# Kernel optimization log

Hardware: AMD Instinct MI355X
Metric: run time of the kernel (lower is better)

Reference implementation:

```python
import jax, jax.numpy as jnp
import numpy as np
import math

D_MODEL = 512
NUM_HEADS = 8
B, L = 2, 4096
EPS_NORM = 1e-8
PLASTICITY = 1.0


def setup_inputs() -> dict:
    key = jax.random.key(0)
    ks = jax.random.split(key, 6)
    D, H = D_MODEL, NUM_HEADS
    std = 1.0 / math.sqrt(D)
    x = jax.random.normal(ks[0], (B, L, D), dtype=jnp.float32)
    qkv_w = jax.random.normal(ks[1], (3 * D, D), dtype=jnp.float32) * std
    qkv_b = jnp.zeros((3 * D,), dtype=jnp.float32)
    out_w = jax.random.normal(ks[2], (D, D), dtype=jnp.float32) * std
    out_b = jnp.zeros((D,), dtype=jnp.float32)
    decay_w = jax.random.normal(ks[3], (H, D), dtype=jnp.float32) * 0.02
    decay_b = jnp.full((H,), 4.0, dtype=jnp.float32)
    norm_scale = jnp.ones((D,), dtype=jnp.float32)
    return {"x": x, "qkv_w": qkv_w, "qkv_b": qkv_b, "out_w": out_w,
            "out_b": out_b, "decay_w": decay_w, "decay_b": decay_b,
            "norm_scale": norm_scale}


def _hebbian_forward(x, qkv_w, qkv_b, out_w, out_b, decay_w, decay_b, norm_scale):
    Bsz, Lsz, D = x.shape
    H = NUM_HEADS
    E = D // H
    # QKV projection (torch Linear: y = x @ W.T + b)
    qkv = x @ qkv_w.T + qkv_b
    q, k, v = jnp.split(qkv, 3, axis=-1)
    q = q.reshape(Bsz, Lsz, H, E)
    k = k.reshape(Bsz, Lsz, H, E)
    v = v.reshape(Bsz, Lsz, H, E)
    # feature map: elu(x) + 1
    q = (jax.nn.elu(q) + 1.0) / math.sqrt(E)
    k = jax.nn.elu(k) + 1.0
    # input-dependent decay per head
    decay_logits = x @ decay_w.T + decay_b          # (B,L,H)
    lambdas = (0.9 + 0.1 * jax.nn.sigmoid(decay_logits)) * PLASTICITY
    log_lambdas = jnp.log(jnp.clip(lambdas, 1e-6))[..., None]   # (B,L,H,1)
    log_lambda_cum = jnp.clip(jnp.cumsum(log_lambdas, axis=1), -50.0, 50.0)
    decay_k = jnp.exp(-log_lambda_cum)
    decay_q = jnp.exp(log_lambda_cum)
    k_decayed = k * decay_k
    q_decayed = q * decay_q
    # outer-product memory state cumsum: (B,L,H,E,E)
    kv = jnp.einsum('blhe,blhf->blhef', k_decayed, v)
    memory_state = jnp.cumsum(kv, axis=1)
    k_sum_decayed = jnp.cumsum(k_decayed, axis=1)
    num = jnp.einsum('blhe,blhef->blhf', q_decayed, memory_state)
    den = jnp.einsum('blhe,blhe->blh', q_decayed, k_sum_decayed)[..., None] + 1e-6
    out = (num / den).reshape(Bsz, Lsz, D)
    out = out @ out_w.T + out_b
    # RMSNorm (dropout is identity in eval)
    rnorm = jax.lax.rsqrt(jnp.mean(out * out, axis=-1, keepdims=True) + EPS_NORM)
    return out * rnorm * norm_scale


def reference(x, qkv_w, qkv_b, out_w, out_b, decay_w, decay_b, norm_scale):
    return _hebbian_forward(x, qkv_w, qkv_b, out_w, out_b, decay_w, decay_b, norm_scale)
```

## Files before the change

### kernel.cpp

```cpp
#include <hip/hip_runtime.h>

typedef unsigned short u16;
typedef unsigned int u32;

#define B_ 2
#define L_ 4096
#define D_ 512
#define H_ 8
#define E_ 64
#define M_ (B_*L_)
#define TD (3*D_)
#define NCH (L_/64)
#define BH (B_*H_)

typedef short bf16x8 __attribute__((ext_vector_type(8)));
typedef float f32x4 __attribute__((ext_vector_type(4)));

__device__ __forceinline__ float bf2f(u16 u){ return __uint_as_float(((u32)u)<<16); }
__device__ __forceinline__ u16 f2bf(float f){
  u32 u = __float_as_uint(f);
  u32 r = u + 0x7FFFu + ((u>>16)&1u);
  return (u16)(r>>16);
}
__device__ __forceinline__ float elu1(float v){ return v>0.f ? v+1.f : __expf(v); }

__device__ __forceinline__ void async_ld16(const u16* g, u16* l){
  __builtin_amdgcn_global_load_lds(
      (const __attribute__((address_space(1))) void*)g,
      (__attribute__((address_space(3))) void*)l, 16, 0, 0);
}

__global__ __launch_bounds__(256) void decay_conv_kernel(const float* __restrict__ x,
    const float* __restrict__ dw, const float* __restrict__ db,
    const float* __restrict__ qw, const float* __restrict__ ow,
    float* __restrict__ ll, u16* __restrict__ xb,
    u16* __restrict__ qwb, u16* __restrict__ owb)
{
  int blk = blockIdx.x;
  if (blk < 2048){
    int wv = threadIdx.x>>6, lane = threadIdx.x&63;
    int m = ((blk&7)<<10) + ((blk>>3)<<2) + wv;
    float xr[8];
    #pragma unroll
    for (int i=0;i<8;i++) xr[i] = x[(size_t)m*D_ + lane + 64*i];
    #pragma unroll
    for (int i=0;i<8;i++) xb[(size_t)m*D_ + lane + 64*i] = f2bf(xr[i]);
    int b = m >> 12, l = m & (L_-1);
    float acc8[8];
    #pragma unroll
    for (int h=0; h<8; h++){
      float a = 0.f;
      #pragma unroll
      for (int i=0;i<8;i++) a += xr[i]*dw[h*D_ + lane + 64*i];
      acc8[h] = a;
    }
    float s4[4];
    #pragma unroll
    for (int i=0;i<4;i++){
      float a = acc8[2*i], bb = acc8[2*i+1];
      bool odd = lane & 1;
      float keep = odd ? bb : a;
      float send = odd ? a : bb;
      s4[i] = keep + __shfl_xor(send, 1);
    }
    float s2[2];
    #pragma unroll
    for (int j=0;j<2;j++){
      float a = s4[2*j], bb = s4[2*j+1];
      bool sel = (lane>>1) & 1;
      float keep = sel ? bb : a;
      float send = sel ? a : bb;
      s2[j] = keep + __shfl_xor(send, 2);
    }
    float r;
    {
      bool sel = (lane>>2) & 1;
      float keep = sel ? s2[1] : s2[0];
      float send = sel ? s2[0] : s2[1];
      r = keep + __shfl_xor(send, 4);
    }
    r += __shfl_xor(r, 8);
    r += __shfl_xor(r, 16);
    r += __shfl_xor(r, 32);
    if (lane < 8){
      float z = r + db[lane];
      float lam = 0.9f + 0.1f/(1.f + __expf(-z));
      ll[((b*H_+lane)*L_) + l] = __logf(lam);
    }
  } else {
    int gid = (blk-2048)*256 + threadIdx.x;
    const float* src; u16* dst; int off;
    if (gid < 196608){ src = qw; dst = qwb; off = gid; }
    else { src = ow; dst = owb; off = gid - 196608; }
    float4 v = ((const float4*)src)[off];
    ushort4 o; o.x=f2bf(v.x); o.y=f2bf(v.y); o.z=f2bf(v.z); o.w=f2bf(v.w);
    ((ushort4*)dst)[off] = o;
  }
}

__global__ __launch_bounds__(256) void scan_kernel(const float* __restrict__ ll,
    float* __restrict__ cb)
{
  int bh = blockIdx.x, t = threadIdx.x;
  int lane = t & 63, wv = t >> 6;
  const float* p = ll + (size_t)bh*L_ + t*16;
  float s[16];
  #pragma unroll
  for (int q=0;q<4;q++){
    float4 v = *(const float4*)(p + q*4);
    s[q*4+0]=v.x; s[q*4+1]=v.y; s[q*4+2]=v.z; s[q*4+3]=v.w;
  }
  #pragma unroll
  for (int i=1;i<16;i++) s[i] += s[i-1];
  float tot = s[15];
  float ws = tot;
  #pragma unroll
  for (int off=1; off<64; off<<=1){
    float tmp = __shfl_up(ws, off);
    if (lane >= off) ws += tmp;
  }
  __shared__ float wsum[4];
  if (lane == 63) wsum[wv] = ws;
  __syncthreads();
  float base = 0.f;
  #pragma unroll
  for (int w2=0; w2<3; w2++) if (w2 < wv) base += wsum[w2];
  float ex = base + ws - tot;
  float* c = cb + (size_t)bh*L_ + t*16;
  #pragma unroll
  for (int i=0;i<16;i++) c[i] = fminf(50.f, fmaxf(-50.f, ex + s[i]));
}

__global__ __launch_bounds__(256) void gemm_qkv_fused(const u16* __restrict__ A,
    const u16* __restrict__ W, const float* __restrict__ bias,
    const float* __restrict__ cb,
    u16* __restrict__ qc, u16* __restrict__ kc, u16* __restrict__ vc)
{
  __shared__ u16 SM[24576];
  const int K = 512;
  int bid0 = blockIdx.x;
  int xcd = bid0 & 7, idx = bid0 >> 3;
  int mblk = xcd*8 + idx/12;
  int nblk = idx % 12;
  int n0 = nblk*128, m0 = mblk*128;
  int t = threadIdx.x, wave = t>>6, lane = t&63;
  int wm = (wave>>1)*64, wn = (wave&1)*64;
  f32x4 acc[4][4] = {};
  int srow = wave*32 + (lane>>2);
  int scol = (lane&3)*8;
  const u16* gA = A + (size_t)(m0+srow)*K + scol;
  const u16* gB = W + (size_t)(n0+srow)*K + scol;
  int q8 = (lane>>4)*8, r16 = lane&15;
  auto STAGE = [&](u16* buf, int k0){
    u16* lA = buf + wave*1024;
    u16* lB = buf + 4096 + wave*1024;
    async_ld16(gA + k0,                lA);
    async_ld16(gA + k0 + 16*(size_t)K, lA + 512);
    async_ld16(gB + k0,                lB);
    async_ld16(gB + k0 + 16*(size_t)K, lB + 512);
  };
  u16 *cB = SM, *nB = SM + 8192, *tB = SM + 16384;
  STAGE(cB, 0);
  STAGE(nB, 32);
  for (int k0=0; k0<K; k0+=32){
    if (k0 + 32 < K) asm volatile("s_waitcnt vmcnt(4)" ::: "memory");
    else             asm volatile("s_waitcnt vmcnt(0)" ::: "memory");
    __builtin_amdgcn_s_barrier();
    if (k0 + 64 < K) STAGE(tB, k0 + 64);
    bf16x8 af[4], bfr[4];
    #pragma unroll
    for (int i=0;i<4;i++) af[i]  = *(const bf16x8*)&cB[(wm + i*16 + r16)*32 + q8];
    #pragma unroll
    for (int j=0;j<4;j++) bfr[j] = *(const bf16x8*)&cB[4096 + (wn + j*16 + r16)*32 + q8];
    #pragma unroll
    for (int i=0;i<4;i++)
      #pragma unroll
      for (int j=0;j<4;j++)
        acc[i][j] = __builtin_amdgcn_mfma_f32_16x16x32_bf16(af[i], bfr[j], acc[i][j], 0,0,0);
    u16* tmp = cB; cB = nB; nB = tB; tB = tmp;
  }
  __syncthreads();
  int g = lane>>4;
  #pragma unroll
  for (int j=0;j<4;j++){
    int col = wn + j*16 + r16;
    float bv = bias[n0 + col];
    #pragma unroll
    for (int i=0;i<4;i++){
      int rbase = wm + i*16 + g*4;
      #pragma unroll
      for (int r=0;r<4;r++)
        SM[(rbase+r)*136 + col] = f2bf(acc[i][j][r] + bv);
    }
  }
  __syncthreads();
  int sec = n0 >> 9;
  #pragma unroll
  for (int u=0;u<8;u++){
    int idx2 = t + 256*u;
    int rloc = idx2 >> 4;
    int colg = (idx2 & 15) * 8;
    int row = m0 + rloc;
    int nn = (n0 + colg) & 511;
    int h2 = nn>>6, e0 = nn&63;
    int bh2 = ((row>>12)<<3) | h2;
    int bid = (bh2<<6) | ((row>>6)&63);
    int l6 = row & 63;
    union { uint4 v; u16 s[8]; } dat;
    dat.v = *(const uint4*)&SM[rloc*136 + colg];
    size_t a = ((size_t)(bid*2 + (e0>>5)))*2048 + (size_t)l6*32 + (e0&31);
    if (sec == 0){
      float eqc = __expf(cb[((size_t)bh2<<12) | (row & 4095)])*0.125f;
      #pragma unroll
      for (int jj=0;jj<8;jj++) dat.s[jj] = f2bf(elu1(bf2f(dat.s[jj]))*eqc);
      *(uint4*)(qc + a) = dat.v;
    } else if (sec == 1){
      float ekc = __expf(-cb[((size_t)bh2<<12) | (row & 4095)]);
      #pragma unroll
      for (int jj=0;jj<8;jj++) dat.s[jj] = f2bf(elu1(bf2f(dat.s[jj]))*ekc);
      *(uint4*)(kc + a) = dat.v;
    } else {
      *(uint4*)(vc + a) = dat.v;
    }
  }
}

__device__ __forceinline__ int chunk_bid_remap(int i){
  int xcd = i & 7;
  int b = xcd >> 2, chhi = xcd & 3;
  int idx = i >> 3;
  int h = idx >> 4, chlo = idx & 15;
  int ch = (chhi<<4) | chlo;
  return (((b<<3)|h)<<6) | ch;
}

__global__ __launch_bounds__(256) void chunk_sums_kernel(const u16* __restrict__ kc,
    const u16* __restrict__ vc, u16* __restrict__ Stc, float* __restrict__ ksc)
{
  int bid = chunk_bid_remap(blockIdx.x);
  __shared__ u16 Kc[4096], Vc[4096];
  __shared__ u16 Ktl[5120], Vtl[5120];
  __shared__ float ksr[256];
  int t = threadIdx.x, w = t>>6, lane = t&63;
  {
    const u16* gk = kc + (size_t)bid*4096 + w*1024 + lane*8;
    const u16* gv = vc + (size_t)bid*4096 + w*1024 + lane*8;
    async_ld16(gk,       Kc + w*1024);
    async_ld16(gk + 512, Kc + w*1024 + 512);
    async_ld16(gv,       Vc + w*1024);
    async_ld16(gv + 512, Vc + w*1024 + 512);
  }
  __syncthreads();
  int e = t & 63, jq = t >> 6;
  {
    u16 kv[16] __attribute__((aligned(16)));
    u16 vv[16] __attribute__((aligned(16)));
    float ksum = 0.f;
    #pragma unroll
    for (int jj=0;jj<16;jj++){
      int j = jq*16+jj;
      kv[jj] = Kc[(e>>5)*2048 + j*32 + (e&31)];
      ksum += bf2f(kv[jj]);
      vv[jj] = Vc[(e>>5)*2048 + j*32 + (e&31)];
    }
    int kh2 = jq>>1, jl = (jq&1)*16;
    u16* kt = &Ktl[(kh2*64 + e)*40 + jl];
    u16* vt = &Vtl[(kh2*64 + e)*40 + jl];
    *(uint4*)kt     = *(const uint4*)&kv[0];
    *(uint4*)(kt+8) = *(const uint4*)&kv[8];
    *(uint4*)vt     = *(const uint4*)&vv[0];
    *(uint4*)(vt+8) = *(const uint4*)&vv[8];
    ksr[t] = ksum;
  }
  __syncthreads();
  int r16 = lane & 15, q8 = (lane>>4)*8;
  bf16x8 av[2];
  #pragma unroll
  for (int kh=0;kh<2;kh++)
    av[kh] = *(const bf16x8*)&Vtl[(kh*64 + w*16 + r16)*40 + q8];
  f32x4 acc[4] = {};
  #pragma unroll
  for (int et=0;et<4;et++)
    #pragma unroll
    for (int kh=0;kh<2;kh++){
      bf16x8 bv = *(const bf16x8*)&Ktl[(kh*64 + et*16 + r16)*40 + q8];
      acc[et] = __builtin_amdgcn_mfma_f32_16x16x32_bf16(av[kh], bv, acc[et], 0,0,0);
    }
  #pragma unroll
  for (int et=0;et<4;et++){
    int eh = et>>1, el = (et&1)*16 + r16;
    #pragma unroll
    for (int r=0;r<4;r++){
      int f = w*16 + (lane>>4)*4 + r;
      Stc[((size_t)bid*2 + eh)*2048 + f*32 + el] = f2bf(acc[et][r]);
    }
  }
  if (t < 64) ksc[bid*64 + t] = ksr[t] + ksr[64+t] + ksr[128+t] + ksr[192+t];
}

__global__ __launch_bounds__(256) void chunk_prefix_kernel(u16* __restrict__ Stc,
    float* __restrict__ ksc)
{
  int blk = blockIdx.x, t = threadIdx.x;
  if (blk < 128){
    int gid = blk*256 + t;
    int bh = gid >> 11, e2 = gid & 2047;
    u32* p = (u32*)Stc + (size_t)bh*131072 + e2;
    float r0 = 0.f, r1 = 0.f;
    #pragma unroll 16
    for (int ch=0; ch<NCH; ch++){
      u32 v = p[ch*2048];
      float lo = bf2f((u16)(v & 0xffffu));
      float hi = bf2f((u16)(v >> 16));
      p[ch*2048] = (u32)f2bf(r0) | ((u32)f2bf(r1) << 16);
      r0 += lo; r1 += hi;
    }
  } else {
    int gid2 = (blk-128)*256 + t;
    int bh2 = gid2 >> 6, e = gid2 & 63;
    float* kp = ksc + bh2*4096 + e;
    float kr = 0.f;
    #pragma unroll 8
    for (int ch=0; ch<NCH; ch++){
      float v = kp[ch*64]; kp[ch*64] = kr; kr += v;
    }
  }
}

__global__ __launch_bounds__(256) void chunk_out_kernel(const u16* __restrict__ qc,
    const u16* __restrict__ kc, const u16* __restrict__ vc,
    const u16* __restrict__ Stc, const float* __restrict__ ksc,
    u16* __restrict__ attn)
{
  int bid = chunk_bid_remap(blockIdx.x);
  int bh = bid >> 6, ch = bid & 63;
  int b = bh >> 3, h = bh & 7;
  __shared__ u16 Kb_l[4096];
  __shared__ u16 Vc_l[4096];
  __shared__ u16 Vt[5120];
  __shared__ u16 Ab[4096];
  __shared__ float R2[320];
  int t = threadIdx.x, w = t>>6, lane = t&63;
  size_t mbase = (size_t)b*L_ + ch*64;
  {
    const u16* gk = kc  + (size_t)bid*4096 + w*1024 + lane*8;
    const u16* gv = vc  + (size_t)bid*4096 + w*1024 + lane*8;
    async_ld16(gk,       Kb_l + w*1024);
    async_ld16(gk + 512, Kb_l + w*1024 + 512);
    async_ld16(gv,       Vc_l + w*1024);
    async_ld16(gv + 512, Vc_l + w*1024 + 512);
  }
  int r16 = lane & 15, q8 = (lane>>4)*8;
  const u16* qg = qc  + (size_t)bid*4096;
  const u16* sg = Stc + (size_t)bid*4096;
  bf16x8 aq[2], sfr[2][4];
  #pragma unroll
  for (int eh=0;eh<2;eh++){
    aq[eh] = *(const bf16x8*)(qg + eh*2048 + (w*16 + r16)*32 + q8);
    #pragma unroll
    for (int ft=0;ft<4;ft++)
      sfr[eh][ft] = *(const bf16x8*)(sg + (eh*64 + ft*16 + r16)*32 + q8);
  }
  int l4 = t>>2, q4 = t&3;
  int ehd = q4>>1, el0 = (q4&1)*16;
  bf16x8 x1 = *(const bf16x8*)(qg + ehd*2048 + l4*32 + el0);
  bf16x8 x2 = *(const bf16x8*)(qg + ehd*2048 + l4*32 + el0 + 8);
  union { float4 v[4]; float f[16]; } kp;
  #pragma unroll
  for (int qq=0;qq<4;qq++)
    kp.v[qq] = *(const float4*)(ksc + bid*64 + q4*16 + qq*4);
  __syncthreads();
  {
    int e = t & 63, jq = t >> 6;
    u16 vv[16] __attribute__((aligned(16)));
    #pragma unroll
    for (int jj=0;jj<16;jj++)
      vv[jj] = Vc_l[(e>>5)*2048 + (jq*16+jj)*32 + (e&31)];
    int jh = jq>>1, jl = (jq&1)*16;
    u16* vt = &Vt[(jh*64 + e)*40 + jl];
    *(uint4*)vt     = *(const uint4*)&vv[0];
    *(uint4*)(vt+8) = *(const uint4*)&vv[8];
  }
  f32x4 accA[4] = {};
  #pragma unroll
  for (int jt=0;jt<4;jt++)
    #pragma unroll
    for (int eh=0;eh<2;eh++){
      bf16x8 bv = *(const bf16x8*)&Kb_l[(eh*64 + jt*16 + r16)*32 + q8];
      accA[jt] = __builtin_amdgcn_mfma_f32_16x16x32_bf16(aq[eh], bv, accA[jt], 0,0,0);
    }
  float dkp = 0.f;
  #pragma unroll
  for (int i=0;i<8;i++)
    dkp += bf2f((u16)x1[i])*kp.f[i] + bf2f((u16)x2[i])*kp.f[8+i];
  #pragma unroll
  for (int jt=0;jt<4;jt++)
    #pragma unroll
    for (int r=0;r<4;r++){
      int lr = w*16 + ((lane>>4)<<2) + r;
      int j  = jt*16 + r16;
      Ab[((jt>>1)*64 + lr)*32 + (jt&1)*16 + r16] = (j <= lr) ? f2bf(accA[jt][r]) : (u16)0;
    }
  __syncthreads();
  float dA = 0.f;
  {
    int jh2 = q4>>1, jl0 = (q4&1)*16;
    bf16x8 y1 = *(const bf16x8*)&Ab[(jh2*64 + l4)*32 + jl0];
    bf16x8 y2 = *(const bf16x8*)&Ab[(jh2*64 + l4)*32 + jl0 + 8];
    #pragma unroll
    for (int i=0;i<8;i++) dA += bf2f((u16)y1[i]) + bf2f((u16)y2[i]);
  }
  R2[t] = dkp + dA;
  __syncthreads();
  if (t < 64) R2[256+t] = R2[t*4] + R2[t*4+1] + R2[t*4+2] + R2[t*4+3] + 1e-6f;
  bf16x8 aA[2];
  #pragma unroll
  for (int jh=0;jh<2;jh++)
    aA[jh] = *(const bf16x8*)&Ab[(jh*64 + w*16 + r16)*32 + q8];
  f32x4 acc[4] = {};
  #pragma unroll
  for (int ft=0;ft<4;ft++){
    #pragma unroll
    for (int jh=0;jh<2;jh++){
      bf16x8 bv = *(const bf16x8*)&Vt[(jh*64 + ft*16 + r16)*40 + q8];
      acc[ft] = __builtin_amdgcn_mfma_f32_16x16x32_bf16(aA[jh], bv, acc[ft], 0,0,0);
    }
    #pragma unroll
    for (int eh=0;eh<2;eh++)
      acc[ft] = __builtin_amdgcn_mfma_f32_16x16x32_bf16(aq[eh], sfr[eh][ft], acc[ft], 0,0,0);
  }
  __syncthreads();
  float inv[4];
  #pragma unroll
  for (int r=0;r<4;r++) inv[r] = 1.f / R2[256 + w*16 + ((lane>>4)<<2) + r];
  #pragma unroll
  for (int ft=0;ft<4;ft++)
    #pragma unroll
    for (int r=0;r<4;r++){
      int lr = w*16 + ((lane>>4)<<2) + r;
      attn[(mbase + lr)*D_ + h*64 + ft*16 + r16] = f2bf(acc[ft][r]*inv[r]);
    }
}

__global__ __launch_bounds__(256) void gemm_rms_kernel(const u16* __restrict__ A,
    const u16* __restrict__ W, const float* __restrict__ bias,
    const float* __restrict__ gnorm, float* __restrict__ out)
{
  __shared__ u16 As[2][1024];
  __shared__ u16 Bs[2][16384];
  __shared__ float ssq_l[4][32];
  __shared__ float rinv_l[32];
  int m0 = blockIdx.x*32;
  int t = threadIdx.x, wave = t>>6, lane = t&63;
  int wn = wave*128;
  int r16 = lane&15, q8 = (lane>>4)*8;
  f32x4 acc[2][8] = {};
  int scol = (t&3)*8;
  const u16* gB = W + (size_t)(t>>2)*512 + scol;
  const u16* gA = A + (size_t)(m0 + (t>>2))*512 + scol;
  {
    if (wave < 2) async_ld16(gA, As[0] + wave*512);
    #pragma unroll
    for (int it=0; it<8; it++)
      async_ld16(gB + it*32768, Bs[0] + wave*512 + it*2048);
  }
  int cur = 0;
  for (int k0=0; k0<512; k0+=32){
    asm volatile("s_waitcnt vmcnt(0)" ::: "memory");
    __builtin_amdgcn_s_barrier();
    if (k0 < 480){
      if (wave < 2) async_ld16(gA + k0+32, As[cur^1] + wave*512);
      #pragma unroll
      for (int it=0; it<8; it++)
        async_ld16(gB + k0+32 + it*32768, Bs[cur^1] + wave*512 + it*2048);
    }
    bf16x8 af0 = *(const bf16x8*)&As[cur][r16*32 + q8];
    bf16x8 af1 = *(const bf16x8*)&As[cur][(16 + r16)*32 + q8];
    #pragma unroll
    for (int j=0;j<8;j++){
      bf16x8 bv = *(const bf16x8*)&Bs[cur][(wn + j*16 + r16)*32 + q8];
      acc[0][j] = __builtin_amdgcn_mfma_f32_16x16x32_bf16(af0, bv, acc[0][j], 0,0,0);
      acc[1][j] = __builtin_amdgcn_mfma_f32_16x16x32_bf16(af1, bv, acc[1][j], 0,0,0);
    }
    cur ^= 1;
  }
  int g = lane>>4;
  float bv8[8], gv8[8];
  #pragma unroll
  for (int j=0;j<8;j++){ int col = wn + j*16 + r16; bv8[j] = bias[col]; gv8[j] = gnorm[col]; }
  float ssq[2][4] = {};
  #pragma unroll
  for (int i=0;i<2;i++)
    #pragma unroll
    for (int j=0;j<8;j++)
      #pragma unroll
      for (int r=0;r<4;r++){
        float v = acc[i][j][r] + bv8[j];
        acc[i][j][r] = v;
        ssq[i][r] += v*v;
      }
  #pragma unroll
  for (int off=1; off<16; off<<=1)
    #pragma unroll
    for (int i=0;i<2;i++)
      #pragma unroll
      for (int r=0;r<4;r++)
        ssq[i][r] += __shfl_xor(ssq[i][r], off);
  if (r16 == 0){
    #pragma unroll
    for (int i=0;i<2;i++)
      #pragma unroll
      for (int r=0;r<4;r++)
        ssq_l[wave][i*16 + g*4 + r] = ssq[i][r];
  }
  __syncthreads();
  if (t < 32)
    rinv_l[t] = rsqrtf((ssq_l[0][t]+ssq_l[1][t]+ssq_l[2][t]+ssq_l[3][t])*(1.f/512.f) + 1e-8f);
  __syncthreads();
  #pragma unroll
  for (int i=0;i<2;i++)
    #pragma unroll
    for (int r=0;r<4;r++){
      int row = m0 + i*16 + g*4 + r;
      float ri = rinv_l[i*16 + g*4 + r];
      #pragma unroll
      for (int j=0;j<8;j++)
        out[(size_t)row*512 + wn + j*16 + r16] = acc[i][j][r]*ri*gv8[j];
    }
}

extern "C" void kernel_launch(void* const* d_in, const int* in_sizes, int n_in,
                              void* d_out, int out_size, void* d_ws, size_t ws_size,
                              hipStream_t stream)
{
  const float* x     = (const float*)d_in[0];
  const float* w_qkv = (const float*)d_in[1];
  const float* b_qkv = (const float*)d_in[2];
  const float* w_out = (const float*)d_in[3];
  const float* b_out = (const float*)d_in[4];
  const float* w_dec = (const float*)d_in[5];
  const float* b_dec = (const float*)d_in[6];
  const float* gnorm = (const float*)d_in[7];
  float* out = (float*)d_out;

  char* ws = (char*)d_ws;
  u16*   qc   = (u16*)(ws);
  u16*   kc   = (u16*)(ws + 8388608);
  u16*   vc   = (u16*)(ws + 16777216);
  u16*   Stc  = (u16*)(ws + 25165824);
  float* ksc  = (float*)(ws + 33554432);
  float* ll   = (float*)(ws + 33816576);
  float* cb   = (float*)(ws + 34078720);
  u16*   xb   = (u16*)(ws + 34340864);
  u16*   qwb  = (u16*)(ws + 42729472);
  u16*   owb  = (u16*)(ws + 44302336);
  u16*   attn = xb;

  decay_conv_kernel<<<dim3(3072), dim3(256), 0, stream>>>(x, w_dec, b_dec, w_qkv, w_out,
                                                          ll, xb, qwb, owb);
  scan_kernel<<<dim3(BH), dim3(256), 0, stream>>>(ll, cb);
  gemm_qkv_fused<<<dim3(768), dim3(256), 0, stream>>>(xb, qwb, b_qkv, cb, qc, kc, vc);
  chunk_sums_kernel<<<dim3(BH*NCH), dim3(256), 0, stream>>>(kc, vc, Stc, ksc);
  chunk_prefix_kernel<<<dim3(132), dim3(256), 0, stream>>>(Stc, ksc);
  chunk_out_kernel<<<dim3(BH*NCH), dim3(256), 0, stream>>>(qc, kc, vc, Stc, ksc, attn);
  gemm_rms_kernel<<<dim3(M_/32), dim3(256), 0, stream>>>(attn, owb, b_out, gnorm, out);
}
```

Before: 150.7 us.

## Load GEMM operands directly from global into registers, dropping LDS staging

Both the QKV GEMM and the output-projection+RMSNorm GEMM stop staging A/B tiles through shared memory with async loads and barriers. Each wave now loads its MFMA fragments straight from global memory into registers, with one-step register double buffering and a fully unrolled K loop. This removes LDS traffic and the block-wide barriers, but each wave re-reads data its neighbours also need, so global/L2 traffic rises. The loads are also less coalesced (16-byte chunks from rows 1 KB apart) and register pressure goes up.

```diff
diff --git a/kernel.cpp b/kernel.cpp
--- a/kernel.cpp
+++ b/kernel.cpp
@@ -136,7 +136,7 @@
     const float* __restrict__ cb,
     u16* __restrict__ qc, u16* __restrict__ kc, u16* __restrict__ vc)
 {
-  __shared__ u16 SM[24576];
+  __shared__ u16 SM[17408];
   const int K = 512;
   int bid0 = blockIdx.x;
   int xcd = bid0 & 7, idx = bid0 >> 3;
@@ -145,41 +145,36 @@
   int n0 = nblk*128, m0 = mblk*128;
   int t = threadIdx.x, wave = t>>6, lane = t&63;
   int wm = (wave>>1)*64, wn = (wave&1)*64;
+  int q8 = (lane>>4)*8, r16 = lane&15;
   f32x4 acc[4][4] = {};
-  int srow = wave*32 + (lane>>2);
-  int scol = (lane&3)*8;
-  const u16* gA = A + (size_t)(m0+srow)*K + scol;
-  const u16* gB = W + (size_t)(n0+srow)*K + scol;
-  int q8 = (lane>>4)*8, r16 = lane&15;
-  auto STAGE = [&](u16* buf, int k0){
-    u16* lA = buf + wave*1024;
-    u16* lB = buf + 4096 + wave*1024;
-    async_ld16(gA + k0,                lA);
-    async_ld16(gA + k0 + 16*(size_t)K, lA + 512);
-    async_ld16(gB + k0,                lB);
-    async_ld16(gB + k0 + 16*(size_t)K, lB + 512);
-  };
-  u16 *cB = SM, *nB = SM + 8192, *tB = SM + 16384;
-  STAGE(cB, 0);
-  STAGE(nB, 32);
+  const u16* pA = A + (size_t)(m0+wm+r16)*K + q8;
+  const u16* pB = W + (size_t)(n0+wn+r16)*K + q8;
+  bf16x8 afc[4], bfc[4];
+  #pragma unroll
+  for (int i=0;i<4;i++){
+    afc[i] = *(const bf16x8*)(pA + (size_t)i*16*K);
+    bfc[i] = *(const bf16x8*)(pB + (size_t)i*16*K);
+  }
+  #pragma unroll
   for (int k0=0; k0<K; k0+=32){
-    if (k0 + 32 < K) asm volatile("s_waitcnt vmcnt(4)" ::: "memory");
-    else             asm volatile("s_waitcnt vmcnt(0)" ::: "memory");
-    __builtin_amdgcn_s_barrier();
-    if (k0 + 64 < K) STAGE(tB, k0 + 64);
-    bf16x8 af[4], bfr[4];
-    #pragma unroll
-    for (int i=0;i<4;i++) af[i]  = *(const bf16x8*)&cB[(wm + i*16 + r16)*32 + q8];
-    #pragma unroll
-    for (int j=0;j<4;j++) bfr[j] = *(const bf16x8*)&cB[4096 + (wn + j*16 + r16)*32 + q8];
+    bf16x8 afn[4], bfn[4];
+    if (k0 + 32 < K){
+      #pragma unroll
+      for (int i=0;i<4;i++){
+        afn[i] = *(const bf16x8*)(pA + (size_t)i*16*K + k0 + 32);
+        bfn[i] = *(const bf16x8*)(pB + (size_t)i*16*K + k0 + 32);
+      }
+    }
     #pragma unroll
     for (int i=0;i<4;i++)
       #pragma unroll
       for (int j=0;j<4;j++)
-        acc[i][j] = __builtin_amdgcn_mfma_f32_16x16x32_bf16(af[i], bfr[j], acc[i][j], 0,0,0);
-    u16* tmp = cB; cB = nB; nB = tB; tB = tmp;
-  }
-  __syncthreads();
+        acc[i][j] = __builtin_amdgcn_mfma_f32_16x16x32_bf16(afc[i], bfc[j], acc[i][j], 0,0,0);
+    if (k0 + 32 < K){
+      #pragma unroll
+      for (int i=0;i<4;i++){ afc[i] = afn[i]; bfc[i] = bfn[i]; }
+    }
+  }
   int g = lane>>4;
   #pragma unroll
   for (int j=0;j<4;j++){
@@ -446,8 +441,6 @@
     const u16* __restrict__ W, const float* __restrict__ bias,
     const float* __restrict__ gnorm, float* __restrict__ out)
 {
-  __shared__ u16 As[2][1024];
-  __shared__ u16 Bs[2][16384];
   __shared__ float ssq_l[4][32];
   __shared__ float rinv_l[32];
   int m0 = blockIdx.x*32;
@@ -455,34 +448,32 @@
   int wn = wave*128;
   int r16 = lane&15, q8 = (lane>>4)*8;
   f32x4 acc[2][8] = {};
-  int scol = (t&3)*8;
-  const u16* gB = W + (size_t)(t>>2)*512 + scol;
-  const u16* gA = A + (size_t)(m0 + (t>>2))*512 + scol;
-  {
-    if (wave < 2) async_ld16(gA, As[0] + wave*512);
-    #pragma unroll
-    for (int it=0; it<8; it++)
-      async_ld16(gB + it*32768, Bs[0] + wave*512 + it*2048);
-  }
-  int cur = 0;
+  const u16* pA = A + (size_t)(m0 + r16)*512 + q8;
+  const u16* pB = W + (size_t)(wn + r16)*512 + q8;
+  bf16x8 a0c, a1c, bc[8];
+  a0c = *(const bf16x8*)(pA);
+  a1c = *(const bf16x8*)(pA + 16*512);
+  #pragma unroll
+  for (int j=0;j<8;j++) bc[j] = *(const bf16x8*)(pB + (size_t)j*16*512);
+  #pragma unroll
   for (int k0=0; k0<512; k0+=32){
-    asm volatile("s_waitcnt vmcnt(0)" ::: "memory");
-    __builtin_amdgcn_s_barrier();
-    if (k0 < 480){
-      if (wave < 2) async_ld16(gA + k0+32, As[cur^1] + wave*512);
-      #pragma unroll
-      for (int it=0; it<8; it++)
-        async_ld16(gB + k0+32 + it*32768, Bs[cur^1] + wave*512 + it*2048);
-    }
-    bf16x8 af0 = *(const bf16x8*)&As[cur][r16*32 + q8];
-    bf16x8 af1 = *(const bf16x8*)&As[cur][(16 + r16)*32 + q8];
+    bf16x8 a0n, a1n, bn[8];
+    if (k0 + 32 < 512){
+      a0n = *(const bf16x8*)(pA + k0 + 32);
+      a1n = *(const bf16x8*)(pA + 16*512 + k0 + 32);
+      #pragma unroll
+      for (int j=0;j<8;j++) bn[j] = *(const bf16x8*)(pB + (size_t)j*16*512 + k0 + 32);
+    }
     #pragma unroll
     for (int j=0;j<8;j++){
-      bf16x8 bv = *(const bf16x8*)&Bs[cur][(wn + j*16 + r16)*32 + q8];
-      acc[0][j] = __builtin_amdgcn_mfma_f32_16x16x32_bf16(af0, bv, acc[0][j], 0,0,0);
-      acc[1][j] = __builtin_amdgcn_mfma_f32_16x16x32_bf16(af1, bv, acc[1][j], 0,0,0);
-    }
-    cur ^= 1;
+      acc[0][j] = __builtin_amdgcn_mfma_f32_16x16x32_bf16(a0c, bc[j], acc[0][j], 0,0,0);
+      acc[1][j] = __builtin_amdgcn_mfma_f32_16x16x32_bf16(a1c, bc[j], acc[1][j], 0,0,0);
+    }
+    if (k0 + 32 < 512){
+      a0c = a0n; a1c = a1n;
+      #pragma unroll
+      for (int j=0;j<8;j++) bc[j] = bn[j];
+    }
   }
   int g = lane>>4;
   float bv8[8], gv8[8];
```

Result: slower. 185.9 us (+23.4%).

## Retile QKV GEMM to 256x192 blocks with 512 threads and swizzled LDS

Applied to the files above, without the earlier changes.

Replaces the QKV GEMM's 128x128 tiles, 256 threads and triple-buffered BK=32 pipeline with 256x192 tiles, 512 threads, double-buffered BK=64 loads and XOR-swizzled shared-memory layout. It also raises MFMA issue priority around the compute loop. The aim is more data reuse per tile, fewer LDS bank conflicts and fewer blocks. In exchange it uses more shared memory and registers per block, and the grid of 256 blocks may underfill the GPU. The epilogue is generalized so one tile can span the q/k/v section boundary.

```diff
diff --git a/kernel.cpp b/kernel.cpp
--- a/kernel.cpp
+++ b/kernel.cpp
@@ -131,84 +131,108 @@
   for (int i=0;i<16;i++) c[i] = fminf(50.f, fmaxf(-50.f, ex + s[i]));
 }
 
-__global__ __launch_bounds__(256) void gemm_qkv_fused(const u16* __restrict__ A,
+#define BUFU 28672
+#define CTS 216
+
+__global__ __launch_bounds__(512, 2) void gemm_qkv_fused(const u16* __restrict__ A,
     const u16* __restrict__ W, const float* __restrict__ bias,
     const float* __restrict__ cb,
     u16* __restrict__ qc, u16* __restrict__ kc, u16* __restrict__ vc)
 {
-  __shared__ u16 SM[24576];
-  const int K = 512;
+  __shared__ u16 SM[57344];
   int bid0 = blockIdx.x;
   int xcd = bid0 & 7, idx = bid0 >> 3;
-  int mblk = xcd*8 + idx/12;
-  int nblk = idx % 12;
-  int n0 = nblk*128, m0 = mblk*128;
+  int mblk = xcd*4 + (idx>>3);
+  int nblk = idx & 7;
+  int m0 = mblk*256, n0 = nblk*192;
   int t = threadIdx.x, wave = t>>6, lane = t&63;
-  int wm = (wave>>1)*64, wn = (wave&1)*64;
-  f32x4 acc[4][4] = {};
-  int srow = wave*32 + (lane>>2);
-  int scol = (lane&3)*8;
-  const u16* gA = A + (size_t)(m0+srow)*K + scol;
-  const u16* gB = W + (size_t)(n0+srow)*K + scol;
-  int q8 = (lane>>4)*8, r16 = lane&15;
-  auto STAGE = [&](u16* buf, int k0){
-    u16* lA = buf + wave*1024;
-    u16* lB = buf + 4096 + wave*1024;
-    async_ld16(gA + k0,                lA);
-    async_ld16(gA + k0 + 16*(size_t)K, lA + 512);
-    async_ld16(gB + k0,                lB);
-    async_ld16(gB + k0 + 16*(size_t)K, lB + 512);
+  int wm = (wave>>2)*128, wn = (wave&3)*48;
+  int r16 = lane&15, q8h = (lane>>4);
+  f32x4 acc[8][3] = {};
+  int srow = t>>3, sslot = t&7;
+  auto STAGE = [&](int kt, int buf){
+    u16* base = SM + buf*BUFU;
+    #pragma unroll
+    for (int r=0;r<4;r++){
+      int row = r*64 + srow;
+      const u16* src = A + (size_t)(m0+row)*512 + kt*64 + ((sslot ^ (row&7))<<3);
+      async_ld16(src, base + r*4096 + t*8);
+    }
+    #pragma unroll
+    for (int r=0;r<3;r++){
+      int row = r*64 + srow;
+      const u16* src = W + (size_t)(n0+row)*512 + kt*64 + ((sslot ^ (row&7))<<3);
+      async_ld16(src, base + 16384 + r*4096 + t*8);
+    }
   };
-  u16 *cB = SM, *nB = SM + 8192, *tB = SM + 16384;
-  STAGE(cB, 0);
-  STAGE(nB, 32);
-  for (int k0=0; k0<K; k0+=32){
-    if (k0 + 32 < K) asm volatile("s_waitcnt vmcnt(4)" ::: "memory");
-    else             asm volatile("s_waitcnt vmcnt(0)" ::: "memory");
+  STAGE(0, 0);
+  for (int kt=0; kt<8; kt++){
+    int buf = kt & 1;
+    if (kt < 7){
+      STAGE(kt+1, buf^1);
+      asm volatile("s_waitcnt vmcnt(7)" ::: "memory");
+    } else {
+      asm volatile("s_waitcnt vmcnt(0)" ::: "memory");
+    }
     __builtin_amdgcn_s_barrier();
-    if (k0 + 64 < K) STAGE(tB, k0 + 64);
-    bf16x8 af[4], bfr[4];
-    #pragma unroll
-    for (int i=0;i<4;i++) af[i]  = *(const bf16x8*)&cB[(wm + i*16 + r16)*32 + q8];
-    #pragma unroll
-    for (int j=0;j<4;j++) bfr[j] = *(const bf16x8*)&cB[4096 + (wn + j*16 + r16)*32 + q8];
-    #pragma unroll
-    for (int i=0;i<4;i++)
-      #pragma unroll
-      for (int j=0;j<4;j++)
-        acc[i][j] = __builtin_amdgcn_mfma_f32_16x16x32_bf16(af[i], bfr[j], acc[i][j], 0,0,0);
-    u16* tmp = cB; cB = nB; nB = tB; tB = tmp;
-  }
-  __syncthreads();
+    const u16* Ab_ = SM + buf*BUFU;
+    const u16* Bb_ = SM + buf*BUFU + 16384;
+    bf16x8 bf[3][2];
+    #pragma unroll
+    for (int n=0;n<3;n++)
+      #pragma unroll
+      for (int ks=0;ks<2;ks++){
+        int row = wn + n*16 + r16;
+        int slot = (ks*4 + q8h) ^ (row&7);
+        bf[n][ks] = *(const bf16x8*)&Bb_[row*64 + slot*8];
+      }
+    __builtin_amdgcn_s_setprio(1);
+    #pragma unroll
+    for (int m=0;m<8;m++){
+      int row = wm + m*16 + r16;
+      int s0 = q8h ^ (row&7);
+      int s1 = (4 + q8h) ^ (row&7);
+      bf16x8 a0 = *(const bf16x8*)&Ab_[row*64 + s0*8];
+      bf16x8 a1 = *(const bf16x8*)&Ab_[row*64 + s1*8];
+      #pragma unroll
+      for (int n=0;n<3;n++){
+        acc[m][n] = __builtin_amdgcn_mfma_f32_16x16x32_bf16(a0, bf[n][0], acc[m][n], 0,0,0);
+        acc[m][n] = __builtin_amdgcn_mfma_f32_16x16x32_bf16(a1, bf[n][1], acc[m][n], 0,0,0);
+      }
+    }
+    __builtin_amdgcn_s_setprio(0);
+    __builtin_amdgcn_s_barrier();
+  }
   int g = lane>>4;
   #pragma unroll
-  for (int j=0;j<4;j++){
-    int col = wn + j*16 + r16;
+  for (int n=0;n<3;n++){
+    int col = wn + n*16 + r16;
     float bv = bias[n0 + col];
     #pragma unroll
-    for (int i=0;i<4;i++){
-      int rbase = wm + i*16 + g*4;
+    for (int m=0;m<8;m++){
+      int rb = wm + m*16 + g*4;
       #pragma unroll
       for (int r=0;r<4;r++)
-        SM[(rbase+r)*136 + col] = f2bf(acc[i][j][r] + bv);
-    }
-  }
-  __syncthreads();
-  int sec = n0 >> 9;
-  #pragma unroll
-  for (int u=0;u<8;u++){
-    int idx2 = t + 256*u;
-    int rloc = idx2 >> 4;
-    int colg = (idx2 & 15) * 8;
+        SM[(rb+r)*CTS + col] = f2bf(acc[m][n][r] + bv);
+    }
+  }
+  __syncthreads();
+  #pragma unroll
+  for (int u=0;u<12;u++){
+    int idx2 = t + 512*u;
+    int rloc = idx2 / 24;
+    int colg = (idx2 % 24) * 8;
     int row = m0 + rloc;
-    int nn = (n0 + colg) & 511;
+    int nc = n0 + colg;
+    int sec = nc >> 9;
+    int nn = nc & 511;
     int h2 = nn>>6, e0 = nn&63;
     int bh2 = ((row>>12)<<3) | h2;
-    int bid = (bh2<<6) | ((row>>6)&63);
+    int bidc = (bh2<<6) | ((row>>6)&63);
     int l6 = row & 63;
     union { uint4 v; u16 s[8]; } dat;
-    dat.v = *(const uint4*)&SM[rloc*136 + colg];
-    size_t a = ((size_t)(bid*2 + (e0>>5)))*2048 + (size_t)l6*32 + (e0&31);
+    dat.v = *(const uint4*)&SM[rloc*CTS + colg];
+    size_t a = ((size_t)(bidc*2 + (e0>>5)))*2048 + (size_t)l6*32 + (e0&31);
     if (sec == 0){
       float eqc = __expf(cb[((size_t)bh2<<12) | (row & 4095)])*0.125f;
       #pragma unroll
@@ -559,7 +583,7 @@
   decay_conv_kernel<<<dim3(3072), dim3(256), 0, stream>>>(x, w_dec, b_dec, w_qkv, w_out,
                                                           ll, xb, qwb, owb);
   scan_kernel<<<dim3(BH), dim3(256), 0, stream>>>(ll, cb);
-  gemm_qkv_fused<<<dim3(768), dim3(256), 0, stream>>>(xb, qwb, b_qkv, cb, qc, kc, vc);
+  gemm_qkv_fused<<<dim3(256), dim3(512), 0, stream>>>(xb, qwb, b_qkv, cb, qc, kc, vc);
   chunk_sums_kernel<<<dim3(BH*NCH), dim3(256), 0, stream>>>(kc, vc, Stc, ksc);
   chunk_prefix_kernel<<<dim3(132), dim3(256), 0, stream>>>(Stc, ksc);
   chunk_out_kernel<<<dim3(BH*NCH), dim3(256), 0, stream>>>(qc, kc, vc, Stc, ksc, attn);
```

After: 153.1 us. About the same (+1.6%).

## Vectorize decay loads, move weight conversion into scan kernel, stage attn stores via LDS

Applied to the files above, without the earlier changes.

The decay kernel now has each lane load and store 8 contiguous floats with float4/uint4 accesses instead of strided scalar accesses. The weight bf16 conversion moves out of the decay kernel and runs alongside the 16-block scan in a combined kernel, so the scan no longer executes almost alone on the GPU. The chunk output kernel writes its results to shared memory first and then emits 16-byte coalesced rows to the attn buffer. This adds an extra LDS round trip and a barrier in the output kernel, and it relies on the Ab buffer being free at that point.

```diff
diff --git a/kernel.cpp b/kernel.cpp
--- a/kernel.cpp
+++ b/kernel.cpp
@@ -32,63 +32,104 @@
 
 __global__ __launch_bounds__(256) void decay_conv_kernel(const float* __restrict__ x,
     const float* __restrict__ dw, const float* __restrict__ db,
-    const float* __restrict__ qw, const float* __restrict__ ow,
-    float* __restrict__ ll, u16* __restrict__ xb,
+    float* __restrict__ ll, u16* __restrict__ xb)
+{
+  int blk = blockIdx.x;
+  int wv = threadIdx.x>>6, lane = threadIdx.x&63;
+  int m = ((blk&7)<<10) + ((blk>>3)<<2) + wv;
+  float xr[8];
+  {
+    float4 v0 = *(const float4*)&x[(size_t)m*D_ + lane*8];
+    float4 v1 = *(const float4*)&x[(size_t)m*D_ + lane*8 + 4];
+    xr[0]=v0.x; xr[1]=v0.y; xr[2]=v0.z; xr[3]=v0.w;
+    xr[4]=v1.x; xr[5]=v1.y; xr[6]=v1.z; xr[7]=v1.w;
+  }
+  {
+    union { uint4 v; u16 s[8]; } o;
+    #pragma unroll
+    for (int i=0;i<8;i++) o.s[i] = f2bf(xr[i]);
+    *(uint4*)&xb[(size_t)m*D_ + lane*8] = o.v;
+  }
+  int b = m >> 12, l = m & (L_-1);
+  float acc8[8];
+  #pragma unroll
+  for (int h=0; h<8; h++){
+    const float4* dp = (const float4*)&dw[h*D_ + lane*8];
+    float4 w0 = dp[0], w1 = dp[1];
+    acc8[h] = xr[0]*w0.x + xr[1]*w0.y + xr[2]*w0.z + xr[3]*w0.w
+            + xr[4]*w1.x + xr[5]*w1.y + xr[6]*w1.z + xr[7]*w1.w;
+  }
+  float s4[4];
+  #pragma unroll
+  for (int i=0;i<4;i++){
+    float a = acc8[2*i], bb = acc8[2*i+1];
+    bool odd = lane & 1;
+    float keep = odd ? bb : a;
+    float send = odd ? a : bb;
+    s4[i] = keep + __shfl_xor(send, 1);
+  }
+  float s2[2];
+  #pragma unroll
+  for (int j=0;j<2;j++){
+    float a = s4[2*j], bb = s4[2*j+1];
+    bool sel = (lane>>1) & 1;
+    float keep = sel ? bb : a;
+    float send = sel ? a : bb;
+    s2[j] = keep + __shfl_xor(send, 2);
+  }
+  float r;
+  {
+    bool sel = (lane>>2) & 1;
+    float keep = sel ? s2[1] : s2[0];
+    float send = sel ? s2[0] : s2[1];
+    r = keep + __shfl_xor(send, 4);
+  }
+  r += __shfl_xor(r, 8);
+  r += __shfl_xor(r, 16);
+  r += __shfl_xor(r, 32);
+  if (lane < 8){
+    float z = r + db[lane];
+    float lam = 0.9f + 0.1f/(1.f + __expf(-z));
+    ll[((b*H_+lane)*L_) + l] = __logf(lam);
+  }
+}
+
+__global__ __launch_bounds__(256) void scan_conv_kernel(const float* __restrict__ ll,
+    float* __restrict__ cb, const float* __restrict__ qw, const float* __restrict__ ow,
     u16* __restrict__ qwb, u16* __restrict__ owb)
 {
-  int blk = blockIdx.x;
-  if (blk < 2048){
-    int wv = threadIdx.x>>6, lane = threadIdx.x&63;
-    int m = ((blk&7)<<10) + ((blk>>3)<<2) + wv;
-    float xr[8];
-    #pragma unroll
-    for (int i=0;i<8;i++) xr[i] = x[(size_t)m*D_ + lane + 64*i];
-    #pragma unroll
-    for (int i=0;i<8;i++) xb[(size_t)m*D_ + lane + 64*i] = f2bf(xr[i]);
-    int b = m >> 12, l = m & (L_-1);
-    float acc8[8];
-    #pragma unroll
-    for (int h=0; h<8; h++){
-      float a = 0.f;
-      #pragma unroll
-      for (int i=0;i<8;i++) a += xr[i]*dw[h*D_ + lane + 64*i];
-      acc8[h] = a;
-    }
-    float s4[4];
-    #pragma unroll
-    for (int i=0;i<4;i++){
-      float a = acc8[2*i], bb = acc8[2*i+1];
-      bool odd = lane & 1;
-      float keep = odd ? bb : a;
-      float send = odd ? a : bb;
-      s4[i] = keep + __shfl_xor(send, 1);
-    }
-    float s2[2];
-    #pragma unroll
-    for (int j=0;j<2;j++){
-      float a = s4[2*j], bb = s4[2*j+1];
-      bool sel = (lane>>1) & 1;
-      float keep = sel ? bb : a;
-      float send = sel ? a : bb;
-      s2[j] = keep + __shfl_xor(send, 2);
-    }
-    float r;
-    {
-      bool sel = (lane>>2) & 1;
-      float keep = sel ? s2[1] : s2[0];
-      float send = sel ? s2[0] : s2[1];
-      r = keep + __shfl_xor(send, 4);
-    }
-    r += __shfl_xor(r, 8);
-    r += __shfl_xor(r, 16);
-    r += __shfl_xor(r, 32);
-    if (lane < 8){
-      float z = r + db[lane];
-      float lam = 0.9f + 0.1f/(1.f + __expf(-z));
-      ll[((b*H_+lane)*L_) + l] = __logf(lam);
-    }
+  int blk = blockIdx.x, t = threadIdx.x;
+  if (blk < BH){
+    int bh = blk;
+    int lane = t & 63, wv = t >> 6;
+    const float* p = ll + (size_t)bh*L_ + t*16;
+    float s[16];
+    #pragma unroll
+    for (int q=0;q<4;q++){
+      float4 v = *(const float4*)(p + q*4);
+      s[q*4+0]=v.x; s[q*4+1]=v.y; s[q*4+2]=v.z; s[q*4+3]=v.w;
+    }
+    #pragma unroll
+    for (int i=1;i<16;i++) s[i] += s[i-1];
+    float tot = s[15];
+    float ws = tot;
+    #pragma unroll
+    for (int off=1; off<64; off<<=1){
+      float tmp = __shfl_up(ws, off);
+      if (lane >= off) ws += tmp;
+    }
+    __shared__ float wsum[4];
+    if (lane == 63) wsum[wv] = ws;
+    __syncthreads();
+    float base = 0.f;
+    #pragma unroll
+    for (int w2=0; w2<3; w2++) if (w2 < wv) base += wsum[w2];
+    float ex = base + ws - tot;
+    float* c = cb + (size_t)bh*L_ + t*16;
+    #pragma unroll
+    for (int i=0;i<16;i++) c[i] = fminf(50.f, fmaxf(-50.f, ex + s[i]));
   } else {
-    int gid = (blk-2048)*256 + threadIdx.x;
+    int gid = (blk-BH)*256 + t;
     const float* src; u16* dst; int off;
     if (gid < 196608){ src = qw; dst = qwb; off = gid; }
     else { src = ow; dst = owb; off = gid - 196608; }
@@ -96,39 +137,6 @@
     ushort4 o; o.x=f2bf(v.x); o.y=f2bf(v.y); o.z=f2bf(v.z); o.w=f2bf(v.w);
     ((ushort4*)dst)[off] = o;
   }
-}
-
-__global__ __launch_bounds__(256) void scan_kernel(const float* __restrict__ ll,
-    float* __restrict__ cb)
-{
-  int bh = blockIdx.x, t = threadIdx.x;
-  int lane = t & 63, wv = t >> 6;
-  const float* p = ll + (size_t)bh*L_ + t*16;
-  float s[16];
-  #pragma unroll
-  for (int q=0;q<4;q++){
-    float4 v = *(const float4*)(p + q*4);
-    s[q*4+0]=v.x; s[q*4+1]=v.y; s[q*4+2]=v.z; s[q*4+3]=v.w;
-  }
-  #pragma unroll
-  for (int i=1;i<16;i++) s[i] += s[i-1];
-  float tot = s[15];
-  float ws = tot;
-  #pragma unroll
-  for (int off=1; off<64; off<<=1){
-    float tmp = __shfl_up(ws, off);
-    if (lane >= off) ws += tmp;
-  }
-  __shared__ float wsum[4];
-  if (lane == 63) wsum[wv] = ws;
-  __syncthreads();
-  float base = 0.f;
-  #pragma unroll
-  for (int w2=0; w2<3; w2++) if (w2 < wv) base += wsum[w2];
-  float ex = base + ws - tot;
-  float* c = cb + (size_t)bh*L_ + t*16;
-  #pragma unroll
-  for (int i=0;i<16;i++) c[i] = fminf(50.f, fmaxf(-50.f, ex + s[i]));
 }
 
 __global__ __launch_bounds__(256) void gemm_qkv_fused(const u16* __restrict__ A,
@@ -438,8 +446,14 @@
     #pragma unroll
     for (int r=0;r<4;r++){
       int lr = w*16 + ((lane>>4)<<2) + r;
-      attn[(mbase + lr)*D_ + h*64 + ft*16 + r16] = f2bf(acc[ft][r]*inv[r]);
-    }
+      Ab[lr*64 + ft*16 + r16] = f2bf(acc[ft][r]*inv[r]);
+    }
+  __syncthreads();
+  {
+    int row = t>>2, cg = (t&3)*16;
+    *(uint4*)&attn[(mbase + row)*D_ + h*64 + cg]     = *(const uint4*)&Ab[row*64 + cg];
+    *(uint4*)&attn[(mbase + row)*D_ + h*64 + cg + 8] = *(const uint4*)&Ab[row*64 + cg + 8];
+  }
 }
 
 __global__ __launch_bounds__(256) void gemm_rms_kernel(const u16* __restrict__ A,
@@ -556,9 +570,8 @@
   u16*   owb  = (u16*)(ws + 44302336);
   u16*   attn = xb;
 
-  decay_conv_kernel<<<dim3(3072), dim3(256), 0, stream>>>(x, w_dec, b_dec, w_qkv, w_out,
-                                                          ll, xb, qwb, owb);
-  scan_kernel<<<dim3(BH), dim3(256), 0, stream>>>(ll, cb);
+  decay_conv_kernel<<<dim3(2048), dim3(256), 0, stream>>>(x, w_dec, b_dec, ll, xb);
+  scan_conv_kernel<<<dim3(BH + 1024), dim3(256), 0, stream>>>(ll, cb, w_qkv, w_out, qwb, owb);
   gemm_qkv_fused<<<dim3(768), dim3(256), 0, stream>>>(xb, qwb, b_qkv, cb, qc, kc, vc);
   chunk_sums_kernel<<<dim3(BH*NCH), dim3(256), 0, stream>>>(kc, vc, Stc, ksc);
   chunk_prefix_kernel<<<dim3(132), dim3(256), 0, stream>>>(Stc, ksc);
```

Result: no change. 151.9 us (+0.8%).
